# Kernel tuning notes

Hardware: AMD Instinct MI355X
Metric: run time of the kernel (lower is better)

Reference implementation:

```python
import jax, jax.numpy as jnp
import numpy as np

N = 40000      # nodes
E = 640000     # edges
D = 128        # input_dim == hidden_dim
G = 64         # graphs in batch


def _mk_linear(key, din, dout):
    kw, kb = jax.random.split(key)
    w = jax.random.normal(kw, (din, dout), jnp.float32) / np.sqrt(din)
    b = jax.random.normal(kb, (dout,), jnp.float32) * 0.01
    return w, b


def setup_inputs() -> dict:
    key = jax.random.key(0)
    ks = jax.random.split(key, 12)
    x = jax.random.normal(ks[0], (N, D), jnp.float32)
    edge_attr = jax.random.normal(ks[1], (E, D), jnp.float32)
    edge_index = jax.random.randint(ks[2], (2, E), 0, N, jnp.int32)
    batch = jnp.sort(jax.random.randint(ks[3], (N,), 0, G, jnp.int32))
    inp = {"x": x, "edge_attr": edge_attr, "edge_index": edge_index, "batch": batch}
    # 4 GINE layers, each with a 2-layer MLP (Linear-ReLU-Linear)
    for i in range(4):
        w1, b1 = _mk_linear(ks[4 + 2 * i], D, D)
        w2, b2 = _mk_linear(ks[5 + 2 * i], D, D)
        inp[f"w{i+1}_1"] = w1
        inp[f"b{i+1}_1"] = b1
        inp[f"w{i+1}_2"] = w2
        inp[f"b{i+1}_2"] = b2
    return inp


def _gine_layer(x, src, dst, edge_attr, w1, b1, w2, b2):
    # message: ReLU(x_src + edge_attr), scatter-sum into dst (PyG GINEConv, eps=0)
    msg = jax.nn.relu(x[src] + edge_attr)                      # [E, D]
    agg = jax.ops.segment_sum(msg, dst, num_segments=N)       # [N, D]
    h = x + agg                                                # (1+eps)*x + agg, eps=0
    h = jnp.maximum(h @ w1 + b1, 0.0) @ w2 + b2                # 2-layer MLP
    return h


def reference(x, edge_attr, edge_index, batch,
              w1_1, b1_1, w1_2, b1_2,
              w2_1, b2_1, w2_2, b2_2,
              w3_1, b3_1, w3_2, b3_2,
              w4_1, b4_1, w4_2, b4_2):
    src, dst = edge_index[0], edge_index[1]
    h = x
    params = [(w1_1, b1_1, w1_2, b1_2), (w2_1, b2_1, w2_2, b2_2),
              (w3_1, b3_1, w3_2, b3_2), (w4_1, b4_1, w4_2, b4_2)]
    for (w1, b1, w2, b2) in params:
        h = jax.nn.relu(_gine_layer(h, src, dst, edge_attr, w1, b1, w2, b2))
    # global mean pool over graphs
    sums = jax.ops.segment_sum(h, batch, num_segments=G)                 # [G, D]
    cnts = jax.ops.segment_sum(jnp.ones((N,), h.dtype), batch, num_segments=G)
    return sums / jnp.maximum(cnts, 1.0)[:, None]
```

## Files before the change

### kernel.cpp

```cpp
#include <hip/hip_runtime.h>

#define NN 40000
#define NE 640000
#define DD 128
#define NG 64

typedef float vf4 __attribute__((ext_vector_type(4)));
typedef unsigned short us4 __attribute__((ext_vector_type(4)));
typedef unsigned short us8 __attribute__((ext_vector_type(8)));
typedef short bf16x8 __attribute__((ext_vector_type(8)));
typedef float f32x4 __attribute__((ext_vector_type(4)));

__device__ inline unsigned short f2bf(float f) {
    unsigned int u = __float_as_uint(f);
    return (unsigned short)((u + 0x7fffu + ((u >> 16) & 1u)) >> 16);
}
__device__ inline float bf2f(unsigned short s) {
    return __uint_as_float((unsigned int)s << 16);
}

#define PRE_CVT_BLKS  2500
#define PRE_W_BLKS    512
#define PRE_H_BLKS    2500
#define PRE_BLOCKS    (PRE_CVT_BLKS + PRE_W_BLKS + PRE_H_BLKS)

template <int USE_BF>
__global__ __launch_bounds__(256) void preamble_k(
    const float* __restrict__ x, unsigned short* __restrict__ hB,
    const float* __restrict__ m0, const float* __restrict__ m1,
    const float* __restrict__ m2, const float* __restrict__ m3,
    const float* __restrict__ m4, const float* __restrict__ m5,
    const float* __restrict__ m6, const float* __restrict__ m7,
    unsigned short* __restrict__ whi, unsigned short* __restrict__ wlo,
    const int* __restrict__ dst, int* __restrict__ cnt)
{
    const int bid = blockIdx.x;
    if (bid < PRE_CVT_BLKS) {
        if (!USE_BF) return;
        size_t i = ((size_t)bid * 256 + threadIdx.x) * 8;
        vf4 a = __builtin_nontemporal_load((const vf4*)(x + i));
        vf4 b = __builtin_nontemporal_load((const vf4*)(x + i + 4));
        us4 o0 = {f2bf(a.x), f2bf(a.y), f2bf(a.z), f2bf(a.w)};
        us4 o1 = {f2bf(b.x), f2bf(b.y), f2bf(b.z), f2bf(b.w)};
        *(us4*)(hB + i) = o0;
        *(us4*)(hB + i + 4) = o1;
    } else if (bid < PRE_CVT_BLKS + PRE_W_BLKS) {
        const float* ms[8] = {m0, m1, m2, m3, m4, m5, m6, m7};
        int b = bid - PRE_CVT_BLKS;
        int mat = b >> 6;
        int idx = (b & 63) * 256 + threadIdx.x;
        float v = ms[mat][idx];
        int k = idx >> 7, n = idx & 127;
        unsigned short h = f2bf(v);
        size_t o = ((size_t)mat << 14) + (size_t)n * DD + k;
        whi[o] = h;
        wlo[o] = f2bf(v - bf2f(h));
    } else {
        int e = (bid - PRE_CVT_BLKS - PRE_W_BLKS) * 256 + threadIdx.x;
        if (e < NE) atomicAdd(&cnt[dst[e]], 1);
    }
}

__global__ __launch_bounds__(128) void bsearch_k(const int* __restrict__ batch,
                                                 int* __restrict__ cntG)
{
    __shared__ int st[NG + 1];
    int g = threadIdx.x;
    if (g <= NG) {
        int lo = 0, hi = NN;
        while (lo < hi) {
            int mid = (lo + hi) >> 1;
            if (batch[mid] < g) lo = mid + 1; else hi = mid;
        }
        st[g] = lo;
    }
    __syncthreads();
    if (g < NG) cntG[g] = st[g + 1] - st[g];
}

__global__ __launch_bounds__(1024) void scan_k(const int* __restrict__ cnt,
                                               int* __restrict__ row_ptr,
                                               int* __restrict__ cursor)
{
    __shared__ int sm[1024];
    int t = threadIdx.x;
    int base = t * 40;
    int4 buf[10];
    if (base + 40 <= NN) {
#pragma unroll
        for (int i = 0; i < 10; ++i) buf[i] = ((const int4*)(cnt + base))[i];
    } else {
#pragma unroll
        for (int i = 0; i < 10; ++i) {
            int idx = base + i * 4;
            int4 v = make_int4(0, 0, 0, 0);
            if (idx + 0 < NN) v.x = cnt[idx + 0];
            if (idx + 1 < NN) v.y = cnt[idx + 1];
            if (idx + 2 < NN) v.z = cnt[idx + 2];
            if (idx + 3 < NN) v.w = cnt[idx + 3];
            buf[i] = v;
        }
    }
    int s = 0;
#pragma unroll
    for (int i = 0; i < 10; ++i) s += buf[i].x + buf[i].y + buf[i].z + buf[i].w;
    sm[t] = s;
    __syncthreads();
    for (int off = 1; off < 1024; off <<= 1) {
        int x = (t >= off) ? sm[t - off] : 0;
        __syncthreads();
        sm[t] += x;
        __syncthreads();
    }
    int run = sm[t] - s;
#pragma unroll
    for (int i = 0; i < 10; ++i) {
        int idx = base + i * 4;
        if (idx + 0 < NN) { row_ptr[idx + 0] = run; cursor[idx + 0] = run; run += buf[i].x; }
        if (idx + 1 < NN) { row_ptr[idx + 1] = run; cursor[idx + 1] = run; run += buf[i].y; }
        if (idx + 2 < NN) { row_ptr[idx + 2] = run; cursor[idx + 2] = run; run += buf[i].z; }
        if (idx + 3 < NN) { row_ptr[idx + 3] = run; cursor[idx + 3] = run; run += buf[i].w; }
    }
    if (t == 1023) row_ptr[NN] = run;
}

__global__ __launch_bounds__(256) void fill_k(const int* __restrict__ src,
                                              const int* __restrict__ dst,
                                              int* __restrict__ cursor,
                                              int2* __restrict__ elist,
                                              int* __restrict__ srcA)
{
    int e = blockIdx.x * 256 + threadIdx.x;
    if (e < NE) {
        int d = dst[e];
        int s = src[e];
        int pos = atomicAdd(&cursor[d], 1);
        elist[pos] = make_int2(s, e);
        srcA[pos] = s;
    }
}

template <int L0>
__global__ __launch_bounds__(256) void gather_bf(
    const unsigned short* __restrict__ hb,
    const float* __restrict__ ea, unsigned short* __restrict__ ea_bf,
    const int2* __restrict__ elist, const int* __restrict__ srcA,
    const int* __restrict__ row_ptr, float* __restrict__ agg)
{
    int grp = blockIdx.x * 8 + (threadIdx.x >> 5);
    int lane = threadIdx.x & 31;
    if (grp >= NN) return;
    int beg = row_ptr[grp], end = row_ptr[grp + 1];

    float4 a0 = make_float4(0.f, 0.f, 0.f, 0.f);
    float4 a1 = make_float4(0.f, 0.f, 0.f, 0.f);
    float4 a2 = make_float4(0.f, 0.f, 0.f, 0.f);
    float4 a3 = make_float4(0.f, 0.f, 0.f, 0.f);
    auto edge = [&](float4& acc, int pos) {
        us4 xv, bv;
        if (L0) {
            int2 pr = elist[pos];
            xv = *(const us4*)(hb + (size_t)pr.x * DD + lane * 4);
            vf4 ev = __builtin_nontemporal_load(
                (const vf4*)(ea + (size_t)pr.y * DD + lane * 4));
            bv = (us4){f2bf(ev.x), f2bf(ev.y), f2bf(ev.z), f2bf(ev.w)};
            *(us4*)(ea_bf + (size_t)pos * DD + lane * 4) = bv;
        } else {
            int s = srcA[pos];
            xv = *(const us4*)(hb + (size_t)s * DD + lane * 4);
            bv = __builtin_nontemporal_load(
                (const us4*)(ea_bf + (size_t)pos * DD + lane * 4));
        }
        acc.x += fmaxf(bf2f(xv.x) + bf2f(bv.x), 0.f);
        acc.y += fmaxf(bf2f(xv.y) + bf2f(bv.y), 0.f);
        acc.z += fmaxf(bf2f(xv.z) + bf2f(bv.z), 0.f);
        acc.w += fmaxf(bf2f(xv.w) + bf2f(bv.w), 0.f);
    };
    int pos = beg;
    for (; pos + 4 <= end; pos += 4) {
        edge(a0, pos); edge(a1, pos + 1); edge(a2, pos + 2); edge(a3, pos + 3);
    }
    for (; pos < end; ++pos) edge(a0, pos);

    us4 sv = *(const us4*)(hb + (size_t)grp * DD + lane * 4);
    float4 o;
    o.x = bf2f(sv.x) + (a0.x + a1.x) + (a2.x + a3.x);
    o.y = bf2f(sv.y) + (a0.y + a1.y) + (a2.y + a3.y);
    o.z = bf2f(sv.z) + (a0.z + a1.z) + (a2.z + a3.z);
    o.w = bf2f(sv.w) + (a0.w + a1.w) + (a2.w + a3.w);
    *(float4*)(agg + (size_t)grp * DD + lane * 4) = o;
}

__device__ inline void acc1f(float4& acc, const float* __restrict__ h,
                             const float* __restrict__ ea,
                             int s, int id, int lane)
{
    const float4 xv = *(const float4*)(h + (size_t)s * DD + lane * 4);
    vf4 ev = __builtin_nontemporal_load((const vf4*)(ea + (size_t)id * DD + lane * 4));
    acc.x += fmaxf(xv.x + ev.x, 0.f);
    acc.y += fmaxf(xv.y + ev.y, 0.f);
    acc.z += fmaxf(xv.z + ev.z, 0.f);
    acc.w += fmaxf(xv.w + ev.w, 0.f);
}

__global__ __launch_bounds__(256) void gather_f32(
    const float* __restrict__ h, const float* __restrict__ ea,
    const int* __restrict__ row_ptr, const int2* __restrict__ elist,
    float* __restrict__ agg)
{
    int grp = blockIdx.x * 8 + (threadIdx.x >> 5);
    int lane = threadIdx.x & 31;
    if (grp >= NN) return;
    int beg = row_ptr[grp], end = row_ptr[grp + 1];

    float4 a0 = make_float4(0.f, 0.f, 0.f, 0.f);
    float4 a1 = make_float4(0.f, 0.f, 0.f, 0.f);
    float4 a2 = make_float4(0.f, 0.f, 0.f, 0.f);
    float4 a3 = make_float4(0.f, 0.f, 0.f, 0.f);
    int e = beg;
    for (; e + 4 <= end; e += 4) {
        int2 p0 = elist[e];
        int2 p1 = elist[e + 1];
        int2 p2 = elist[e + 2];
        int2 p3 = elist[e + 3];
        acc1f(a0, h, ea, p0.x, p0.y, lane);
        acc1f(a1, h, ea, p1.x, p1.y, lane);
        acc1f(a2, h, ea, p2.x, p2.y, lane);
        acc1f(a3, h, ea, p3.x, p3.y, lane);
    }
    for (; e < end; ++e) {
        int2 p0 = elist[e];
        acc1f(a0, h, ea, p0.x, p0.y, lane);
    }
    const float4 sv = *(const float4*)(h + (size_t)grp * DD + lane * 4);
    float4 o;
    o.x = sv.x + (a0.x + a1.x) + (a2.x + a3.x);
    o.y = sv.y + (a0.y + a1.y) + (a2.y + a3.y);
    o.z = sv.z + (a0.z + a1.z) + (a2.z + a3.z);
    o.w = sv.w + (a0.w + a1.w) + (a2.w + a3.w);
    *(float4*)(agg + (size_t)grp * DD + lane * 4) = o;
}

template <int MODE>
__global__ __launch_bounds__(256, 2) void mlp_fused(
    const float* __restrict__ A,
    const unsigned short* __restrict__ W1h, const unsigned short* __restrict__ W1l,
    const float* __restrict__ b1v,
    const unsigned short* __restrict__ W2h, const unsigned short* __restrict__ W2l,
    const float* __restrict__ b2v,
    float* C, unsigned short* Cb,
    float* __restrict__ outp, const int* __restrict__ batch)
{
    __shared__ __align__(16) char lds[64 * 1024];
    __shared__ int sbatch[64];
    char* lAh = lds;
    char* lAl = lds + 16 * 1024;
    char* lBh = lds + 32 * 1024;
    char* lBl = lds + 48 * 1024;

    const int tid = threadIdx.x;
    const int m0 = blockIdx.x * 64;

    const int wc  = tid >> 2;
    const int wk0 = (tid & 3) * 32;
    const int wbase = wc * 256 + wk0 * 2;
    const int wsw = (wc & 7) << 4;
    auto stageW = [&](const unsigned short* Wh_, const unsigned short* Wl_,
                      int col0) {
        const unsigned short* sh = Wh_ + (size_t)(col0 + wc) * DD + wk0;
        const unsigned short* sl = Wl_ + (size_t)(col0 + wc) * DD + wk0;
#pragma unroll
        for (int i = 0; i < 4; ++i) {
            const int off = (wbase + i * 16) ^ wsw;
            *(us8*)(lBh + off) = *(const us8*)(sh + i * 8);
            *(us8*)(lBl + off) = *(const us8*)(sl + i * 8);
        }
    };

    {
        const int row = tid >> 2;
        const int c0 = (tid & 3) * 32;
        const float* srcp = A + (size_t)(m0 + row) * DD + c0;
        const int base = row * 256 + c0 * 2;
        const int sw = (row & 7) << 4;
#pragma unroll
        for (int i = 0; i < 4; ++i) {
            float4 v0 = *(const float4*)(srcp + i * 8);
            float4 v1 = *(const float4*)(srcp + i * 8 + 4);
            float f[8] = {v0.x, v0.y, v0.z, v0.w, v1.x, v1.y, v1.z, v1.w};
            us8 hv, lv;
#pragma unroll
            for (int j = 0; j < 8; ++j) {
                unsigned short hb = f2bf(f[j]);
                hv[j] = hb;
                lv[j] = f2bf(f[j] - bf2f(hb));
            }
            const int off = (base + i * 16) ^ sw;
            *(us8*)(lAh + off) = hv;
            *(us8*)(lAl + off) = lv;
        }
    }
    stageW(W1h, W1l, 0);
    __syncthreads();

    const int lane64 = tid & 63;
    const int wid = tid >> 6;
    const int lr = lane64 & 15;
    const int kg = lane64 >> 4;
    const int swr = (lr & 7) << 4;

    bf16x8 ah[4], al[4];
    auto loadA = [&]() {
#pragma unroll
        for (int ks = 0; ks < 4; ++ks) {
            const int off = ((wid * 16 + lr) * 256 + ks * 64 + kg * 16) ^ swr;
            ah[ks] = *(const bf16x8*)(lAh + off);
            al[ks] = *(const bf16x8*)(lAl + off);
        }
    };
    f32x4 acc[8];
    auto mfma_half = [&](int ab) {
#pragma unroll
        for (int nfl = 0; nfl < 4; ++nfl) {
#pragma unroll
            for (int ks = 0; ks < 4; ++ks) {
                const int off = ((nfl * 16 + lr) * 256 + ks * 64 + kg * 16) ^ swr;
                bf16x8 bh = *(const bf16x8*)(lBh + off);
                bf16x8 bl = *(const bf16x8*)(lBl + off);
                acc[ab + nfl] = __builtin_amdgcn_mfma_f32_16x16x32_bf16(ah[ks], bh, acc[ab + nfl], 0, 0, 0);
                acc[ab + nfl] = __builtin_amdgcn_mfma_f32_16x16x32_bf16(ah[ks], bl, acc[ab + nfl], 0, 0, 0);
                acc[ab + nfl] = __builtin_amdgcn_mfma_f32_16x16x32_bf16(al[ks], bh, acc[ab + nfl], 0, 0, 0);
            }
        }
    };

    loadA();
#pragma unroll
    for (int nf = 0; nf < 8; ++nf) acc[nf] = (f32x4){0.f, 0.f, 0.f, 0.f};
    mfma_half(0);
    __syncthreads();
    stageW(W1h, W1l, 64);
    __syncthreads();
    mfma_half(4);
    __syncthreads();

#pragma unroll
    for (int nf = 0; nf < 8; ++nf) {
        const int col = nf * 16 + lr;
        const float b = b1v[col];
#pragma unroll
        for (int r = 0; r < 4; ++r) {
            float u = fmaxf(acc[nf][r] + b, 0.0f);
            const int lrow = wid * 16 + kg * 4 + r;
            const int off = (lrow * 256 + col * 2) ^ ((lrow & 7) << 4);
            unsigned short hb = f2bf(u);
            *(unsigned short*)(lAh + off) = hb;
            *(unsigned short*)(lAl + off) = f2bf(u - bf2f(hb));
        }
    }
    stageW(W2h, W2l, 0);
    __syncthreads();

    loadA();
#pragma unroll
    for (int nf = 0; nf < 8; ++nf) acc[nf] = (f32x4){0.f, 0.f, 0.f, 0.f};
    mfma_half(0);
    __syncthreads();
    stageW(W2h, W2l, 64);
    __syncthreads();
    mfma_half(4);

    if (MODE == 0) {
#pragma unroll
        for (int nf = 0; nf < 8; ++nf) {
            const int col = nf * 16 + lr;
            const float b = b2v[col];
            const size_t rbase = (size_t)(m0 + wid * 16 + kg * 4) * DD + col;
#pragma unroll
            for (int r = 0; r < 4; ++r)
                C[rbase + (size_t)r * DD] = fmaxf(acc[nf][r] + b, 0.0f);
        }
    } else if (MODE == 1) {
#pragma unroll
        for (int nf = 0; nf < 8; ++nf) {
            const int col = nf * 16 + lr;
            const float b = b2v[col];
            const size_t rbase = (size_t)(m0 + wid * 16 + kg * 4) * DD + col;
#pragma unroll
            for (int r = 0; r < 4; ++r)
                Cb[rbase + (size_t)r * DD] = f2bf(fmaxf(acc[nf][r] + b, 0.0f));
        }
    } else {
        float* pstage = (float*)lds;
        if (tid < 64) sbatch[tid] = batch[m0 + tid];
        __syncthreads();
#pragma unroll
        for (int nf = 0; nf < 8; ++nf) {
            const int col = nf * 16 + lr;
            const float b = b2v[col];
            const int row = wid * 16 + kg * 4;
#pragma unroll
            for (int r = 0; r < 4; ++r)
                pstage[(row + r) * DD + col] = fmaxf(acc[nf][r] + b, 0.0f);
        }
        __syncthreads();
        const int col = tid & 127;
        const int row0 = (tid >> 7) * 32;
        float run = 0.f;
        int gprev = sbatch[row0];
        for (int r = row0; r < row0 + 32; ++r) {
            int gg = sbatch[r];
            if (gg != gprev) {
                unsafeAtomicAdd(outp + (size_t)gprev * DD + col, run);
                run = 0.f;
                gprev = gg;
            }
            run += pstage[r * DD + col];
        }
        unsafeAtomicAdd(outp + (size_t)gprev * DD + col, run);
    }
}

__device__ inline void pool_flush(float* __restrict__ out, int g, int lane,
                                  const float4& acc)
{
    float* o = out + (size_t)g * DD + lane * 4;
    unsafeAtomicAdd(o + 0, acc.x);
    unsafeAtomicAdd(o + 1, acc.y);
    unsafeAtomicAdd(o + 2, acc.z);
    unsafeAtomicAdd(o + 3, acc.w);
}

__global__ __launch_bounds__(256) void pool_k(
    const float* __restrict__ h, const int* __restrict__ batch,
    float* __restrict__ out)
{
    int tid = blockIdx.x * 256 + threadIdx.x;
    int grp = tid >> 5;
    int lane = tid & 31;
    int n0 = grp * 16;
    if (n0 >= NN) return;
    int nend = min(n0 + 16, NN);

    float4 acc = make_float4(0.f, 0.f, 0.f, 0.f);
    int gprev = batch[n0];
    for (int n = n0; n < nend; ++n) {
        int g = batch[n];
        if (g != gprev) {
            pool_flush(out, gprev, lane, acc);
            acc = make_float4(0.f, 0.f, 0.f, 0.f);
            gprev = g;
        }
        float4 v = *(const float4*)(h + (size_t)n * DD + lane * 4);
        acc.x += v.x; acc.y += v.y; acc.z += v.z; acc.w += v.w;
    }
    pool_flush(out, gprev, lane, acc);
}

__global__ __launch_bounds__(256) void pool_div_k(float* __restrict__ out,
                                                  const int* __restrict__ cnt)
{
    int tid = blockIdx.x * 256 + threadIdx.x;
    if (tid >= NG * DD) return;
    int g = tid / DD;
    float c = fmaxf((float)cnt[g], 1.0f);
    out[tid] = out[tid] / c;
}

extern "C" void kernel_launch(void* const* d_in, const int* in_sizes, int n_in,
                              void* d_out, int out_size, void* d_ws, size_t ws_size,
                              hipStream_t stream)
{
    const float* x     = (const float*)d_in[0];
    const float* ea    = (const float*)d_in[1];
    const int*   ei    = (const int*)d_in[2];
    const int*   batch = (const int*)d_in[3];
    const float* w1[4], * b1[4], * w2[4], * b2[4];
    for (int l = 0; l < 4; ++l) {
        w1[l] = (const float*)d_in[4 + 4 * l];
        b1[l] = (const float*)d_in[5 + 4 * l];
        w2[l] = (const float*)d_in[6 + 4 * l];
        b2[l] = (const float*)d_in[7 + 4 * l];
    }

    const int* srcp = ei;
    const int* dstp = ei + NE;

    char* ws = (char*)d_ws;
    const size_t hbytes = (size_t)NN * DD * sizeof(float);
    float* agg = (float*)ws;
    float* hA  = (float*)(ws + hbytes);
    char*  p   = ws + 2 * hbytes;
    int*  cnt_node = (int*)p;           p += ((NN * 4 + 255) & ~255);
    int*  row_ptr  = (int*)p;           p += (((NN + 1) * 4 + 255) & ~255);
    int*  cursor   = (int*)p;           p += ((NN * 4 + 255) & ~255);
    int2* elist    = (int2*)p;          p += (((size_t)NE * 8 + 255) & ~255);
    int*  srcA     = (int*)p;           p += (((size_t)NE * 4 + 255) & ~255);
    int*  cntG     = (int*)p;           p += 256;
    unsigned short* wt_hi = (unsigned short*)p;  p += (size_t)8 * 16384 * 2;
    unsigned short* wt_lo = (unsigned short*)p;  p += (size_t)8 * 16384 * 2;
    unsigned short* hB = (unsigned short*)p;     p += (size_t)NN * DD * 2;
    unsigned short* ea_bf = (unsigned short*)p;
    const size_t need_bf = (size_t)(p - ws) + (size_t)NE * DD * 2;
    const bool use_bf = (ws_size >= need_bf);

    const int eblocks     = (NE + 255) / 256;
    const int gblocks     = (NN + 7) / 8;
    const int gemm_blocks = NN / 64;
    const int pool_blocks = ((NN / 16) * 32 + 255) / 256;

    hipMemsetAsync(cnt_node, 0, NN * sizeof(int), stream);
    hipMemsetAsync(d_out, 0, (size_t)NG * DD * sizeof(float), stream);
    if (use_bf)
        preamble_k<1><<<PRE_BLOCKS, 256, 0, stream>>>(
            x, hB, w1[0], w2[0], w1[1], w2[1], w1[2], w2[2], w1[3], w2[3],
            wt_hi, wt_lo, dstp, cnt_node);
    else
        preamble_k<0><<<PRE_BLOCKS, 256, 0, stream>>>(
            x, nullptr, w1[0], w2[0], w1[1], w2[1], w1[2], w2[2], w1[3], w2[3],
            wt_hi, wt_lo, dstp, cnt_node);
    bsearch_k<<<1, 128, 0, stream>>>(batch, cntG);
    scan_k<<<1, 1024, 0, stream>>>(cnt_node, row_ptr, cursor);
    fill_k<<<eblocks, 256, 0, stream>>>(srcp, dstp, cursor, elist, srcA);

    if (use_bf) {
        const unsigned short* wh[8];
        const unsigned short* wl[8];
        for (int m = 0; m < 8; ++m) {
            wh[m] = wt_hi + ((size_t)m << 14);
            wl[m] = wt_lo + ((size_t)m << 14);
        }
        for (int l = 0; l < 4; ++l) {
            if (l == 0)
                gather_bf<1><<<gblocks, 256, 0, stream>>>(
                    hB, ea, ea_bf, elist, nullptr, row_ptr, agg);
            else
                gather_bf<0><<<gblocks, 256, 0, stream>>>(
                    hB, nullptr, ea_bf, nullptr, srcA, row_ptr, agg);
            if (l < 3)
                mlp_fused<1><<<gemm_blocks, 256, 0, stream>>>(
                    agg, wh[2 * l], wl[2 * l], b1[l],
                    wh[2 * l + 1], wl[2 * l + 1], b2[l],
                    nullptr, hB, nullptr, nullptr);
            else
                mlp_fused<2><<<gemm_blocks, 256, 0, stream>>>(
                    agg, wh[2 * l], wl[2 * l], b1[l],
                    wh[2 * l + 1], wl[2 * l + 1], b2[l],
                    nullptr, nullptr, (float*)d_out, batch);
        }
    } else {
        const float* hcur = x;
        for (int l = 0; l < 4; ++l) {
            gather_f32<<<gblocks, 256, 0, stream>>>(hcur, ea, row_ptr, elist, agg);
            const unsigned short* h1  = wt_hi + ((size_t)(2 * l) << 14);
            const unsigned short* lo1 = wt_lo + ((size_t)(2 * l) << 14);
            const unsigned short* h2  = wt_hi + ((size_t)(2 * l + 1) << 14);
            const unsigned short* lo2 = wt_lo + ((size_t)(2 * l + 1) << 14);
            mlp_fused<0><<<gemm_blocks, 256, 0, stream>>>(
                agg, h1, lo1, b1[l], h2, lo2, b2[l], hA, nullptr, nullptr, nullptr);
            hcur = hA;
        }
        pool_k<<<pool_blocks, 256, 0, stream>>>(hA, batch, (float*)d_out);
    }

    pool_div_k<<<(NG * DD + 255) / 256, 256, 0, stream>>>((float*)d_out, cntG);
}
```

Before: 859.2 us.

## Read MLP weights directly from global memory and merge bsearch into scan launch

The fused MLP kernel no longer stages the bf16 hi/lo weight tiles through LDS. Each wave now loads its B fragments straight from global memory, which relies on the L1/L2 caches since every block reads the same 64KB of weights. This halves LDS use to 32KB and drops several barriers, so launch bounds are raised to allow 4 blocks per CU. Separately, the graph-count binary search is folded into the scan kernel as a second block, removing one launch. The risk is higher global and cache load latency on the MFMA inner loop, and the higher occupancy target may cost registers.

```diff
diff --git a/kernel.cpp b/kernel.cpp
--- a/kernel.cpp
+++ b/kernel.cpp
@@ -61,29 +61,30 @@
     }
 }
 
-__global__ __launch_bounds__(128) void bsearch_k(const int* __restrict__ batch,
-                                                 int* __restrict__ cntG)
-{
-    __shared__ int st[NG + 1];
-    int g = threadIdx.x;
-    if (g <= NG) {
-        int lo = 0, hi = NN;
-        while (lo < hi) {
-            int mid = (lo + hi) >> 1;
-            if (batch[mid] < g) lo = mid + 1; else hi = mid;
-        }
-        st[g] = lo;
-    }
-    __syncthreads();
-    if (g < NG) cntG[g] = st[g + 1] - st[g];
-}
-
 __global__ __launch_bounds__(1024) void scan_k(const int* __restrict__ cnt,
                                                int* __restrict__ row_ptr,
-                                               int* __restrict__ cursor)
+                                               int* __restrict__ cursor,
+                                               const int* __restrict__ batch,
+                                               int* __restrict__ cntG)
 {
     __shared__ int sm[1024];
+    __shared__ int st[NG + 1];
     int t = threadIdx.x;
+
+    if (blockIdx.x == 1) {
+        if (t <= NG) {
+            int lo = 0, hi = NN;
+            while (lo < hi) {
+                int mid = (lo + hi) >> 1;
+                if (batch[mid] < t) lo = mid + 1; else hi = mid;
+            }
+            st[t] = lo;
+        }
+        __syncthreads();
+        if (t < NG) cntG[t] = st[t + 1] - st[t];
+        return;
+    }
+
     int base = t * 40;
     int4 buf[10];
     if (base + 40 <= NN) {
@@ -242,7 +243,7 @@
 }
 
 template <int MODE>
-__global__ __launch_bounds__(256, 2) void mlp_fused(
+__global__ __launch_bounds__(256, 4) void mlp_fused(
     const float* __restrict__ A,
     const unsigned short* __restrict__ W1h, const unsigned short* __restrict__ W1l,
     const float* __restrict__ b1v,
@@ -251,31 +252,13 @@
     float* C, unsigned short* Cb,
     float* __restrict__ outp, const int* __restrict__ batch)
 {
-    __shared__ __align__(16) char lds[64 * 1024];
+    __shared__ __align__(16) char lds[32 * 1024];
     __shared__ int sbatch[64];
     char* lAh = lds;
     char* lAl = lds + 16 * 1024;
-    char* lBh = lds + 32 * 1024;
-    char* lBl = lds + 48 * 1024;
 
     const int tid = threadIdx.x;
     const int m0 = blockIdx.x * 64;
-
-    const int wc  = tid >> 2;
-    const int wk0 = (tid & 3) * 32;
-    const int wbase = wc * 256 + wk0 * 2;
-    const int wsw = (wc & 7) << 4;
-    auto stageW = [&](const unsigned short* Wh_, const unsigned short* Wl_,
-                      int col0) {
-        const unsigned short* sh = Wh_ + (size_t)(col0 + wc) * DD + wk0;
-        const unsigned short* sl = Wl_ + (size_t)(col0 + wc) * DD + wk0;
-#pragma unroll
-        for (int i = 0; i < 4; ++i) {
-            const int off = (wbase + i * 16) ^ wsw;
-            *(us8*)(lBh + off) = *(const us8*)(sh + i * 8);
-            *(us8*)(lBl + off) = *(const us8*)(sl + i * 8);
-        }
-    };
 
     {
         const int row = tid >> 2;
@@ -300,7 +283,6 @@
             *(us8*)(lAl + off) = lv;
         }
     }
-    stageW(W1h, W1l, 0);
     __syncthreads();
 
     const int lane64 = tid & 63;
@@ -319,17 +301,18 @@
         }
     };
     f32x4 acc[8];
-    auto mfma_half = [&](int ab) {
-#pragma unroll
-        for (int nfl = 0; nfl < 4; ++nfl) {
+    auto mfma_all = [&](const unsigned short* __restrict__ Wh_,
+                        const unsigned short* __restrict__ Wl_) {
+#pragma unroll
+        for (int nf = 0; nf < 8; ++nf) {
+            const size_t cbase = (size_t)(nf * 16 + lr) * DD + kg * 8;
 #pragma unroll
             for (int ks = 0; ks < 4; ++ks) {
-                const int off = ((nfl * 16 + lr) * 256 + ks * 64 + kg * 16) ^ swr;
-                bf16x8 bh = *(const bf16x8*)(lBh + off);
-                bf16x8 bl = *(const bf16x8*)(lBl + off);
-                acc[ab + nfl] = __builtin_amdgcn_mfma_f32_16x16x32_bf16(ah[ks], bh, acc[ab + nfl], 0, 0, 0);
-                acc[ab + nfl] = __builtin_amdgcn_mfma_f32_16x16x32_bf16(ah[ks], bl, acc[ab + nfl], 0, 0, 0);
-                acc[ab + nfl] = __builtin_amdgcn_mfma_f32_16x16x32_bf16(al[ks], bh, acc[ab + nfl], 0, 0, 0);
+                bf16x8 bh = *(const bf16x8*)(Wh_ + cbase + ks * 32);
+                bf16x8 bl = *(const bf16x8*)(Wl_ + cbase + ks * 32);
+                acc[nf] = __builtin_amdgcn_mfma_f32_16x16x32_bf16(ah[ks], bh, acc[nf], 0, 0, 0);
+                acc[nf] = __builtin_amdgcn_mfma_f32_16x16x32_bf16(ah[ks], bl, acc[nf], 0, 0, 0);
+                acc[nf] = __builtin_amdgcn_mfma_f32_16x16x32_bf16(al[ks], bh, acc[nf], 0, 0, 0);
             }
         }
     };
@@ -337,11 +320,7 @@
     loadA();
 #pragma unroll
     for (int nf = 0; nf < 8; ++nf) acc[nf] = (f32x4){0.f, 0.f, 0.f, 0.f};
-    mfma_half(0);
-    __syncthreads();
-    stageW(W1h, W1l, 64);
-    __syncthreads();
-    mfma_half(4);
+    mfma_all(W1h, W1l);
     __syncthreads();
 
 #pragma unroll
@@ -358,17 +337,12 @@
             *(unsigned short*)(lAl + off) = f2bf(u - bf2f(hb));
         }
     }
-    stageW(W2h, W2l, 0);
     __syncthreads();
 
     loadA();
 #pragma unroll
     for (int nf = 0; nf < 8; ++nf) acc[nf] = (f32x4){0.f, 0.f, 0.f, 0.f};
-    mfma_half(0);
-    __syncthreads();
-    stageW(W2h, W2l, 64);
-    __syncthreads();
-    mfma_half(4);
+    mfma_all(W2h, W2l);
 
     if (MODE == 0) {
 #pragma unroll
@@ -519,8 +493,7 @@
         preamble_k<0><<<PRE_BLOCKS, 256, 0, stream>>>(
             x, nullptr, w1[0], w2[0], w1[1], w2[1], w1[2], w2[2], w1[3], w2[3],
             wt_hi, wt_lo, dstp, cnt_node);
-    bsearch_k<<<1, 128, 0, stream>>>(batch, cntG);
-    scan_k<<<1, 1024, 0, stream>>>(cnt_node, row_ptr, cursor);
+    scan_k<<<2, 1024, 0, stream>>>(cnt_node, row_ptr, cursor, batch, cntG);
     fill_k<<<eblocks, 256, 0, stream>>>(srcp, dstp, cursor, elist, srcA);
 
     if (use_bf) {
```

Result: slower. 957.3 us (+11.4%).
